# Optimization experiments

Hardware: AMD Instinct MI355X
Metric: run time of the kernel (lower is better)

The kernel has to match this reference:

```python
import jax, jax.numpy as jnp
import numpy as np

N_SRC, N_MID, N_DST = 200000, 50000, 10000
D = 128
E1, E2 = 800000, 160000
EPS = 1e-12  # F.normalize eps


def setup_inputs() -> dict:
    key = jax.random.key(0)
    ks = jax.random.split(key, 12)
    s = 1.0 / np.sqrt(D)
    return {
        "x": jax.random.normal(ks[0], (N_SRC, D), jnp.float32),
        "W_l1": jax.random.uniform(ks[1], (D, D), jnp.float32, -s, s),
        "b_l1": jax.random.uniform(ks[2], (D,), jnp.float32, -s, s),
        "W_r1": jax.random.uniform(ks[3], (D, D), jnp.float32, -s, s),
        "W_l2": jax.random.uniform(ks[4], (D, D), jnp.float32, -s, s),
        "b_l2": jax.random.uniform(ks[5], (D,), jnp.float32, -s, s),
        "W_r2": jax.random.uniform(ks[6], (D, D), jnp.float32, -s, s),
        "row1": jax.random.randint(ks[7], (E1,), 0, N_SRC, jnp.int32),
        "col1": jax.random.randint(ks[8], (E1,), 0, N_MID, jnp.int32),
        "row2": jax.random.randint(ks[9], (E2,), 0, N_MID, jnp.int32),
        "col2": jax.random.randint(ks[10], (E2,), 0, N_DST, jnp.int32),
    }


def _sage_conv(x_src, x_dst, row, col, W_l, b_l, W_r, n_dst):
    # mean aggregation of source features over incoming edges (gather + scatter-add)
    msg = x_src[row]                                              # [E, D]
    agg = jax.ops.segment_sum(msg, col, num_segments=n_dst)       # [n_dst, D]
    deg = jax.ops.segment_sum(jnp.ones((row.shape[0],), x_src.dtype), col,
                              num_segments=n_dst)[:, None]        # [n_dst, 1]
    mean = jnp.where(deg > 0, agg / jnp.maximum(deg, 1.0), 0.0)
    out = mean @ W_l.T + b_l + x_dst @ W_r.T                      # lin_l + lin_r (root)
    # L2 normalize (normalize=True)
    norm = jnp.sqrt(jnp.sum(out * out, axis=-1, keepdims=True))
    return out / jnp.maximum(norm, EPS)


def reference(x, W_l1, b_l1, W_r1, W_l2, b_l2, W_r2, row1, col1, row2, col2):
    # layer 1: src = all sampled nodes, dst = first N_MID nodes
    h = _sage_conv(x, x[:N_MID], row1, col1, W_l1, b_l1, W_r1, N_MID)
    h = jax.nn.relu(h)  # dropout is identity in eval mode
    # layer 2: src = mid nodes, dst = first N_DST nodes (the batch targets)
    out = _sage_conv(h, h[:N_DST], row2, col2, W_l2, b_l2, W_r2, N_DST)
    return out
```

## Files before the change

kernel.cpp:

```cpp
#include <hip/hip_runtime.h>
#include <hip/hip_bf16.h>

#define DD 128
#define N_SRC 200000
#define N_MID 50000
#define N_DST 10000
#define E1 800000
#define E2 160000
#define CAP 48

#define BK_W  200
#define NB1   250
#define NB2   50
#define CCAP  3584
#define P1E   2048
#define NP1_1 ((E1 + P1E - 1) / P1E)
#define NP1_2 ((E2 + P1E - 1) / P1E)
#define P1_BLOCKS (NP1_1 + NP1_2)

typedef unsigned short u16;
typedef unsigned int u32;
typedef __attribute__((ext_vector_type(8))) short s16x8;
typedef __attribute__((ext_vector_type(4))) float f32x4;
typedef __attribute__((ext_vector_type(4))) float fv4;


__device__ __forceinline__ float bf_lo(u32 u) {
    union { u32 u; float f; } v; v.u = u << 16; return v.f;
}
__device__ __forceinline__ float bf_hi(u32 u) {
    union { u32 u; float f; } v; v.u = u & 0xffff0000u; return v.f;
}
__device__ __forceinline__ u32 f2bf_bits(float f) {
    union { float f; u32 u; } v; v.f = f;
    return (v.u + 0x7fffu + ((v.u >> 16) & 1u)) >> 16;
}
__device__ __forceinline__ u32 pack2bf(float lo, float hi) {
    return f2bf_bits(lo) | (f2bf_bits(hi) << 16);
}


#define NCONV8 (N_SRC * DD / 8)
#define WTF_T 8192
#define PREP_T (NCONV8 + WTF_T)
#define PREP_BLOCKS ((PREP_T + 255) / 256)
#define PA_BLOCKS (P1_BLOCKS + PREP_BLOCKS)

__global__ __launch_bounds__(256, 8) void prep_part(
    const float* __restrict__ x, u16* __restrict__ xb,
    const float* __restrict__ Wl1, const float* __restrict__ Wr1,
    u16* __restrict__ WTf1,
    const float* __restrict__ Wl2, const float* __restrict__ Wr2,
    u16* __restrict__ WTf2,
    const int* __restrict__ row1, const int* __restrict__ col1,
    const int* __restrict__ row2, const int* __restrict__ col2,
    int* __restrict__ ccnt1, int* __restrict__ ccnt2,
    int2* __restrict__ cbuf1, int2* __restrict__ cbuf2)
{
    __shared__ int lcnt[256];
    __shared__ int gbase[256];
    const int b = blockIdx.x;
    const int tid = threadIdx.x;

    if (b < P1_BLOCKS) {
        const int* __restrict__ colp;
        const int* __restrict__ rowp;
        int* __restrict__ ccnt;
        int2* __restrict__ cbuf;
        int e0, ne, nb;
        if (b < NP1_1) {
            colp = col1; rowp = row1; ccnt = ccnt1; cbuf = cbuf1;
            e0 = b * P1E; ne = E1 - e0; if (ne > P1E) ne = P1E; nb = NB1;
        } else {
            int bb = b - NP1_1;
            colp = col2; rowp = row2; ccnt = ccnt2; cbuf = cbuf2;
            e0 = bb * P1E; ne = E2 - e0; if (ne > P1E) ne = P1E; nb = NB2;
        }
        for (int t = tid; t < nb; t += 256) lcnt[t] = 0;
        __syncthreads();
        int ep[8];
        #pragma unroll
        for (int j = 0; j < 8; ++j) {
            int e = tid + j * 256;
            ep[j] = -1;
            if (e < ne) {
                int c = colp[e0 + e];
                int bk = c / BK_W;
                int rk = atomicAdd(&lcnt[bk], 1);
                ep[j] = (bk << 16) | rk;
            }
        }
        __syncthreads();
        for (int t = tid; t < nb; t += 256) {
            int c = lcnt[t];
            gbase[t] = c ? atomicAdd(&ccnt[t], c) : 0;
        }
        __syncthreads();
        #pragma unroll
        for (int j = 0; j < 8; ++j) {
            if (ep[j] >= 0) {
                int e = e0 + tid + j * 256;
                int bk = ep[j] >> 16;
                int pos = gbase[bk] + (ep[j] & 0xffff);
                if (pos < CCAP)
                    cbuf[(size_t)bk * CCAP + pos] = make_int2(colp[e], rowp[e]);
            }
        }
    } else {
        int i = (b - P1_BLOCKS) * 256 + tid;
        if (i < NCONV8) {
            const fv4* x4 = (const fv4*)x;
            fv4 a = __builtin_nontemporal_load(x4 + i * 2);
            fv4 bb = __builtin_nontemporal_load(x4 + i * 2 + 1);
            uint4 o;
            o.x = pack2bf(a[0], a[1]); o.y = pack2bf(a[2], a[3]);
            o.z = pack2bf(bb[0], bb[1]); o.w = pack2bf(bb[2], bb[3]);
            ((uint4*)xb)[i] = o;
        } else if (i < NCONV8 + WTF_T) {
            int t = i - NCONV8;
            int layer = t >> 12;
            int rem = t & 4095;
            int kt = rem >> 9;
            int nt = (rem >> 6) & 7;
            int lane = rem & 63;
            int gn = nt * 16 + (lane & 15);
            int k0 = kt * 32 + (lane >> 4) * 8;
            const float* Wl = layer ? Wl2 : Wl1;
            const float* Wr = layer ? Wr2 : Wr1;
            u16* WTf = layer ? WTf2 : WTf1;
            u32 o[4];
            #pragma unroll
            for (int p = 0; p < 4; ++p) {
                int ka = k0 + 2 * p, kb = ka + 1;
                float ea = (ka < 128) ? Wl[gn * 128 + ka] : Wr[gn * 128 + (ka - 128)];
                float eb = (kb < 128) ? Wl[gn * 128 + kb] : Wr[gn * 128 + (kb - 128)];
                o[p] = pack2bf(ea, eb);
            }
            ((uint4*)WTf)[(kt * 8 + nt) * 64 + lane] = make_uint4(o[0], o[1], o[2], o[3]);
        }
    }
}


__global__ __launch_bounds__(256, 8) void bucket_sort(
    const int2* __restrict__ cbuf1, const int2* __restrict__ cbuf2,
    const int* __restrict__ ccnt1, const int* __restrict__ ccnt2,
    int* __restrict__ cnt1, int* __restrict__ cnt2,
    int* __restrict__ csr1, int* __restrict__ csr2)
{
    const int b = blockIdx.x;
    const int tid = threadIdx.x;
    const int2* __restrict__ cbuf;
    const int* __restrict__ ccnt;
    int* __restrict__ cnt;
    int* __restrict__ csr;
    int bkt;
    if (b < NB1) { cbuf = cbuf1; ccnt = ccnt1; cnt = cnt1; csr = csr1; bkt = b; }
    else         { cbuf = cbuf2; ccnt = ccnt2; cnt = cnt2; csr = csr2; bkt = b - NB1; }
    const int col0 = bkt * BK_W;

    __shared__ int hist[BK_W];
    for (int t = tid; t < BK_W; t += 256) hist[t] = 0;
    __syncthreads();

    int n = ccnt[bkt]; if (n > CCAP) n = CCAP;
    const int2* bp = cbuf + (size_t)bkt * CCAP;
    for (int e = tid; e < n; e += 512) {
        int2 cr0 = bp[e];
        int e1i = e + 256;
        bool h1 = e1i < n;
        int2 cr1 = h1 ? bp[e1i] : cr0;
        int r0 = atomicAdd(&hist[cr0.x - col0], 1);
        if (r0 < CAP) csr[cr0.x * CAP + r0] = cr0.y;
        if (h1) {
            int r1 = atomicAdd(&hist[cr1.x - col0], 1);
            if (r1 < CAP) csr[cr1.x * CAP + r1] = cr1.y;
        }
    }
    __syncthreads();
    for (int t = tid; t < BK_W; t += 256) cnt[col0 + t] = hist[t];
}


template <int ROWS, bool RELU, int MINB>
__global__ __launch_bounds__(256, MINB) void sage_kernel(
    const u16* __restrict__ xsrc_b, const u16* __restrict__ xdst_b,
    const int* __restrict__ cnt, const int* __restrict__ csrf,
    const u16* __restrict__ WTf, const float* __restrict__ bias,
    float* __restrict__ out_f, u16* __restrict__ out_b,
    int n_dst, int fp32lim)
{
    __shared__ float smem[ROWS * 132];
    const int tid = threadIdx.x;
    const int i0 = blockIdx.x * ROWS;
    const int lane = tid & 63;
    const int w = tid >> 6;
    const int quarter = lane >> 4;
    const int l16 = lane & 15;
    const int half = lane >> 5;
    const int l32 = lane & 31;
    constexpr int RPW = ROWS / 4;

    const uint4* __restrict__ xs4 = (const uint4*)xsrc_b;
    const uint2* __restrict__ xd2 = (const uint2*)xdst_b;
    uint4* sA4 = (uint4*)smem;
    uint2* sA2 = (uint2*)smem;

    int degv = 0;
    {
        int rr = i0 + w * RPW + lane;
        if (lane < RPW && rr < n_dst) degv = cnt[rr];
    }
    int ivA = 0, ivB = 0;
    {
        int iA = i0 + w * RPW;
        if (iA < n_dst)     ivA = csrf[(size_t)iA * CAP + lane];
        if (iA + 1 < n_dst) ivB = csrf[(size_t)(iA + 1) * CAP + lane];
    }

    for (int qq = 0; qq < RPW; qq += 2) {
        int rA = w * RPW + qq, rB = rA + 1;
        int iA = i0 + rA, iB = i0 + rB;
        int degA = __shfl(degv, qq);     if (degA > CAP) degA = CAP;
        int degB = __shfl(degv, qq + 1); if (degB > CAP) degB = CAP;
        int curA = ivA, curB = ivB;
        if (qq + 2 < RPW) {
            int i2 = iA + 2, i3 = iA + 3;
            ivA = (i2 < n_dst) ? csrf[(size_t)i2 * CAP + lane] : 0;
            ivB = (i3 < n_dst) ? csrf[(size_t)i3 * CAP + lane] : 0;
        }
        float accA[8] = {0.f,0.f,0.f,0.f,0.f,0.f,0.f,0.f};
        float accB[8] = {0.f,0.f,0.f,0.f,0.f,0.f,0.f,0.f};
        int dmax = degA > degB ? degA : degB;
        for (int g = 0; g < dmax; g += 16) {
            #pragma unroll
            for (int j = 0; j < 4; ++j) {
                int rel = g + 4 * j + quarter;
                if (g + 4 * j < degA) {
                    int idx = __shfl(curA, rel & 63);
                    float m = (rel < degA) ? 1.f : 0.f;
                    uint4 u = xs4[(size_t)idx * 16 + l16];
                    accA[0] += m * bf_lo(u.x); accA[1] += m * bf_hi(u.x);
                    accA[2] += m * bf_lo(u.y); accA[3] += m * bf_hi(u.y);
                    accA[4] += m * bf_lo(u.z); accA[5] += m * bf_hi(u.z);
                    accA[6] += m * bf_lo(u.w); accA[7] += m * bf_hi(u.w);
                }
                if (g + 4 * j < degB) {
                    int idx = __shfl(curB, rel & 63);
                    float m = (rel < degB) ? 1.f : 0.f;
                    uint4 u = xs4[(size_t)idx * 16 + l16];
                    accB[0] += m * bf_lo(u.x); accB[1] += m * bf_hi(u.x);
                    accB[2] += m * bf_lo(u.y); accB[3] += m * bf_hi(u.y);
                    accB[4] += m * bf_lo(u.z); accB[5] += m * bf_hi(u.z);
                    accB[6] += m * bf_lo(u.w); accB[7] += m * bf_hi(u.w);
                }
            }
        }
        #pragma unroll
        for (int k = 0; k < 8; ++k) {
            accA[k] += __shfl_xor(accA[k], 16);
            accA[k] += __shfl_xor(accA[k], 32);
            accB[k] += __shfl_xor(accB[k], 16);
            accB[k] += __shfl_xor(accB[k], 32);
        }
        float sA = (degA > 0) ? 1.f / (float)degA : 0.f;
        float sB = (degB > 0) ? 1.f / (float)degB : 0.f;
        if (quarter == 0) {
            uint4 oA, oB;
            oA.x = pack2bf(accA[0]*sA, accA[1]*sA); oA.y = pack2bf(accA[2]*sA, accA[3]*sA);
            oA.z = pack2bf(accA[4]*sA, accA[5]*sA); oA.w = pack2bf(accA[6]*sA, accA[7]*sA);
            oB.x = pack2bf(accB[0]*sB, accB[1]*sB); oB.y = pack2bf(accB[2]*sB, accB[3]*sB);
            oB.z = pack2bf(accB[4]*sB, accB[5]*sB); oB.w = pack2bf(accB[6]*sB, accB[7]*sB);
            sA4[rA * 33 + l16] = oA;
            sA4[rB * 33 + l16] = oB;
        }
        if (half == 1) {
            uint2 rootA = (iA < n_dst) ? xd2[(size_t)iA * 32 + l32] : make_uint2(0, 0);
            uint2 rootB = (iB < n_dst) ? xd2[(size_t)iB * 32 + l32] : make_uint2(0, 0);
            sA2[rA * 66 + 32 + l32] = rootA;
            sA2[rB * 66 + 32 + l32] = rootB;
        }
    }
    __syncthreads();

    constexpr int MT = ROWS / 16;
    const int nt0 = w * 2;
    const s16x8* sAv = (const s16x8*)smem;
    const s16x8* Bv = (const s16x8*)WTf;

    f32x4 C[MT][2];
    #pragma unroll
    for (int mt = 0; mt < MT; ++mt)
        #pragma unroll
        for (int ni = 0; ni < 2; ++ni)
            C[mt][ni] = (f32x4){0.f, 0.f, 0.f, 0.f};

    #pragma unroll
    for (int kt = 0; kt < 8; ++kt) {
        s16x8 a[MT];
        #pragma unroll
        for (int mt = 0; mt < MT; ++mt)
            a[mt] = sAv[(mt * 16 + l16) * 33 + kt * 4 + quarter];
        s16x8 b0 = Bv[(kt * 8 + nt0) * 64 + lane];
        s16x8 b1 = Bv[(kt * 8 + nt0 + 1) * 64 + lane];
        #pragma unroll
        for (int mt = 0; mt < MT; ++mt) {
            C[mt][0] = __builtin_amdgcn_mfma_f32_16x16x32_bf16(a[mt], b0, C[mt][0], 0, 0, 0);
            C[mt][1] = __builtin_amdgcn_mfma_f32_16x16x32_bf16(a[mt], b1, C[mt][1], 0, 0, 0);
        }
    }

    __syncthreads();
    float* sOut = smem;

    #pragma unroll
    for (int ni = 0; ni < 2; ++ni) {
        int col = (nt0 + ni) * 16 + l16;
        float bc = bias[col];
        #pragma unroll
        for (int mt = 0; mt < MT; ++mt) {
            #pragma unroll
            for (int r = 0; r < 4; ++r) {
                int row = mt * 16 + quarter * 4 + r;
                sOut[row * 132 + col] = C[mt][ni][r] + bc;
            }
        }
    }
    __syncthreads();

    constexpr int R = ROWS / 8;
    const int ty = tid >> 5;
    const int tx = tid & 31;
    #pragma unroll
    for (int r = 0; r < R; ++r) {
        int row = ty * R + r;
        float4 v = *(const float4*)(&sOut[row * 132 + tx * 4]);
        float s = v.x * v.x + v.y * v.y + v.z * v.z + v.w * v.w;
        #pragma unroll
        for (int off = 1; off < 32; off <<= 1) s += __shfl_xor(s, off);
        float scale = 1.f / fmaxf(sqrtf(s), 1e-12f);
        float v0 = v.x * scale, v1 = v.y * scale, v2 = v.z * scale, v3 = v.w * scale;
        if (RELU) {
            v0 = fmaxf(v0, 0.f); v1 = fmaxf(v1, 0.f);
            v2 = fmaxf(v2, 0.f); v3 = fmaxf(v3, 0.f);
        }
        int i = i0 + row;
        if (i < n_dst) {
            if (i < fp32lim)
                *(float4*)(out_f + (size_t)i * DD + tx * 4) = make_float4(v0, v1, v2, v3);
            if (out_b) {
                uint2 ob;
                ob.x = pack2bf(v0, v1);
                ob.y = pack2bf(v2, v3);
                *(uint2*)(out_b + (size_t)i * DD + tx * 4) = ob;
            }
        }
    }
}


extern "C" void kernel_launch(void* const* d_in, const int* in_sizes, int n_in,
                              void* d_out, int out_size, void* d_ws, size_t ws_size,
                              hipStream_t stream) {
    const float* x    = (const float*)d_in[0];
    const float* Wl1  = (const float*)d_in[1];
    const float* bl1  = (const float*)d_in[2];
    const float* Wr1  = (const float*)d_in[3];
    const float* Wl2  = (const float*)d_in[4];
    const float* bl2  = (const float*)d_in[5];
    const float* Wr2  = (const float*)d_in[6];
    const int* row1   = (const int*)d_in[7];
    const int* col1   = (const int*)d_in[8];
    const int* row2   = (const int*)d_in[9];
    const int* col2   = (const int*)d_in[10];
    float* out = (float*)d_out;

    char* p = (char*)d_ws;
    u16* xb    = (u16*)p;   p += (size_t)N_SRC * DD * sizeof(u16);
    u16* hb    = (u16*)p;   p += (size_t)N_MID * DD * sizeof(u16);
    u16* WTf1  = (u16*)p;   p += (size_t)256 * 128 * sizeof(u16);
    u16* WTf2  = (u16*)p;   p += (size_t)256 * 128 * sizeof(u16);
    int2* cbuf1 = (int2*)p; p += (size_t)NB1 * CCAP * sizeof(int2);
    int2* cbuf2 = (int2*)p; p += (size_t)NB2 * CCAP * sizeof(int2);
    char* zbase = p;
    int* ccnt1 = (int*)p;   p += 256 * sizeof(int);
    int* ccnt2 = (int*)p;   p += 64 * sizeof(int);
    int* cnt1  = (int*)p;   p += (size_t)N_MID * sizeof(int);
    int* cnt2  = (int*)p;   p += (size_t)N_DST * sizeof(int);
    int* csr1  = (int*)p;   p += (size_t)N_MID * CAP * sizeof(int);
    int* csr2  = (int*)p;   p += (size_t)N_DST * CAP * sizeof(int);
    p += 256;
    size_t zlen = (size_t)(p - zbase);

    (void)hipMemsetAsync(zbase, 0, zlen, stream);

    prep_part<<<PA_BLOCKS, 256, 0, stream>>>(
        x, xb, Wl1, Wr1, WTf1, Wl2, Wr2, WTf2,
        row1, col1, row2, col2, ccnt1, ccnt2, cbuf1, cbuf2);

    bucket_sort<<<NB1 + NB2, 256, 0, stream>>>(
        cbuf1, cbuf2, ccnt1, ccnt2, cnt1, cnt2, csr1, csr2);

    sage_kernel<32, true, 4><<<(N_MID + 31) / 32, 256, 0, stream>>>(
        xb, xb, cnt1, csr1, WTf1, bl1, (float*)nullptr, hb, N_MID, 0);

    sage_kernel<16, false, 4><<<(N_DST + 15) / 16, 256, 0, stream>>>(
        hb, hb, cnt2, csr2, WTf2, bl2, out, (u16*)nullptr, N_DST, N_DST);
}
```

Baseline: 251.2 us.

## Shrink workspace memset and fold layer-2 bucket sort into layer-1 SAGE kernel

The workspace memset now clears only the small bucket counters instead of the full cnt/csr arrays (several MB), removing a large zeroing pass. Because csr slots beyond the degree are no longer zeroed, gather indices are clamped to the valid source range so stale data cannot cause out-of-bounds loads. The layer-2 bucket sort now runs as extra blocks at the front of the layer-1 SAGE kernel, so it overlaps with layer-1 aggregation and the separate bucket_sort launch only handles layer 1. The risk is extra per-edge work from the clamp and some imbalance from mixing sort blocks with compute blocks.

```diff
diff --git a/kernel.cpp b/kernel.cpp
--- a/kernel.cpp
+++ b/kernel.cpp
@@ -142,27 +142,13 @@
 }
 
 
-__global__ __launch_bounds__(256, 8) void bucket_sort(
-    const int2* __restrict__ cbuf1, const int2* __restrict__ cbuf2,
-    const int* __restrict__ ccnt1, const int* __restrict__ ccnt2,
-    int* __restrict__ cnt1, int* __restrict__ cnt2,
-    int* __restrict__ csr1, int* __restrict__ csr2)
+__device__ __forceinline__ void sort_bucket(
+    int bkt, const int2* __restrict__ cbuf, const int* __restrict__ ccnt,
+    int* __restrict__ cnt, int* __restrict__ csr, int* hist, int tid)
 {
-    const int b = blockIdx.x;
-    const int tid = threadIdx.x;
-    const int2* __restrict__ cbuf;
-    const int* __restrict__ ccnt;
-    int* __restrict__ cnt;
-    int* __restrict__ csr;
-    int bkt;
-    if (b < NB1) { cbuf = cbuf1; ccnt = ccnt1; cnt = cnt1; csr = csr1; bkt = b; }
-    else         { cbuf = cbuf2; ccnt = ccnt2; cnt = cnt2; csr = csr2; bkt = b - NB1; }
     const int col0 = bkt * BK_W;
-
-    __shared__ int hist[BK_W];
     for (int t = tid; t < BK_W; t += 256) hist[t] = 0;
     __syncthreads();
-
     int n = ccnt[bkt]; if (n > CCAP) n = CCAP;
     const int2* bp = cbuf + (size_t)bkt * CCAP;
     for (int e = tid; e < n; e += 512) {
@@ -182,17 +168,34 @@
 }
 
 
+__global__ __launch_bounds__(256, 8) void bucket_sort(
+    const int2* __restrict__ cbuf1, const int* __restrict__ ccnt1,
+    int* __restrict__ cnt1, int* __restrict__ csr1)
+{
+    __shared__ int hist[BK_W];
+    sort_bucket(blockIdx.x, cbuf1, ccnt1, cnt1, csr1, hist, threadIdx.x);
+}
+
+
 template <int ROWS, bool RELU, int MINB>
 __global__ __launch_bounds__(256, MINB) void sage_kernel(
     const u16* __restrict__ xsrc_b, const u16* __restrict__ xdst_b,
     const int* __restrict__ cnt, const int* __restrict__ csrf,
     const u16* __restrict__ WTf, const float* __restrict__ bias,
     float* __restrict__ out_f, u16* __restrict__ out_b,
-    int n_dst, int fp32lim)
+    int n_dst, int fp32lim, int nsrc,
+    const int2* __restrict__ cbufR, const int* __restrict__ ccntR,
+    int* __restrict__ cntR, int* __restrict__ csrR, int nrole)
 {
     __shared__ float smem[ROWS * 132];
     const int tid = threadIdx.x;
-    const int i0 = blockIdx.x * ROWS;
+
+    if (blockIdx.x < (u32)nrole) {
+        sort_bucket(blockIdx.x, cbufR, ccntR, cntR, csrR, (int*)smem, tid);
+        return;
+    }
+
+    const int i0 = (blockIdx.x - nrole) * ROWS;
     const int lane = tid & 63;
     const int w = tid >> 6;
     const int quarter = lane >> 4;
@@ -238,6 +241,7 @@
                 int rel = g + 4 * j + quarter;
                 if (g + 4 * j < degA) {
                     int idx = __shfl(curA, rel & 63);
+                    idx = ((u32)idx < (u32)nsrc) ? idx : 0;
                     float m = (rel < degA) ? 1.f : 0.f;
                     uint4 u = xs4[(size_t)idx * 16 + l16];
                     accA[0] += m * bf_lo(u.x); accA[1] += m * bf_hi(u.x);
@@ -247,6 +251,7 @@
                 }
                 if (g + 4 * j < degB) {
                     int idx = __shfl(curB, rel & 63);
+                    idx = ((u32)idx < (u32)nsrc) ? idx : 0;
                     float m = (rel < degB) ? 1.f : 0.f;
                     uint4 u = xs4[(size_t)idx * 16 + l16];
                     accB[0] += m * bf_lo(u.x); accB[1] += m * bf_hi(u.x);
@@ -385,12 +390,12 @@
     char* zbase = p;
     int* ccnt1 = (int*)p;   p += 256 * sizeof(int);
     int* ccnt2 = (int*)p;   p += 64 * sizeof(int);
+    size_t zlen = (size_t)(p - zbase);
     int* cnt1  = (int*)p;   p += (size_t)N_MID * sizeof(int);
     int* cnt2  = (int*)p;   p += (size_t)N_DST * sizeof(int);
     int* csr1  = (int*)p;   p += (size_t)N_MID * CAP * sizeof(int);
     int* csr2  = (int*)p;   p += (size_t)N_DST * CAP * sizeof(int);
     p += 256;
-    size_t zlen = (size_t)(p - zbase);
 
     (void)hipMemsetAsync(zbase, 0, zlen, stream);
 
@@ -398,12 +403,13 @@
         x, xb, Wl1, Wr1, WTf1, Wl2, Wr2, WTf2,
         row1, col1, row2, col2, ccnt1, ccnt2, cbuf1, cbuf2);
 
-    bucket_sort<<<NB1 + NB2, 256, 0, stream>>>(
-        cbuf1, cbuf2, ccnt1, ccnt2, cnt1, cnt2, csr1, csr2);
-
-    sage_kernel<32, true, 4><<<(N_MID + 31) / 32, 256, 0, stream>>>(
-        xb, xb, cnt1, csr1, WTf1, bl1, (float*)nullptr, hb, N_MID, 0);
+    bucket_sort<<<NB1, 256, 0, stream>>>(cbuf1, ccnt1, cnt1, csr1);
+
+    sage_kernel<32, true, 4><<<NB2 + (N_MID + 31) / 32, 256, 0, stream>>>(
+        xb, xb, cnt1, csr1, WTf1, bl1, (float*)nullptr, hb, N_MID, 0, N_SRC,
+        cbuf2, ccnt2, cnt2, csr2, NB2);
 
     sage_kernel<16, false, 4><<<(N_DST + 15) / 16, 256, 0, stream>>>(
-        hb, hb, cnt2, csr2, WTf2, bl2, out, (u16*)nullptr, N_DST, N_DST);
-}
+        hb, hb, cnt2, csr2, WTf2, bl2, out, (u16*)nullptr, N_DST, N_DST, N_MID,
+        (const int2*)nullptr, (const int*)nullptr, nullptr, nullptr, 0);
+}
```

After: 253.0 us. About the same (+0.7%).
